# Optimization experiments

Hardware: AMD Instinct MI355X
Metric: run time of the kernel (lower is better)

## Reference

```python
import jax, jax.numpy as jnp
import numpy as np
from jax import lax

DN = ('NCHW', 'OIHW', 'NCHW')

def _edge_bank():
    # All eight fixed stencils embedded in 5x5 (3x3 kernels zero-padded to center),
    # equivalent to the original per-kernel SAME conv. Order matches torch.cat order:
    # sobel_x, sobel_y, diag1, diag2, laplacian, gradient5x5, scharr_x, scharr_y
    k3 = [
        [[-1, 0, 1], [-2, 0, 2], [-1, 0, 1]],            # sobel_x
        [[-1, -2, -1], [0, 0, 0], [1, 2, 1]],            # sobel_y
        [[0, 1, 2], [-1, 0, 1], [-2, -1, 0]],            # diag1
        [[-2, -1, 0], [-1, 0, 1], [0, 1, 2]],            # diag2
        [[0, 1, 0], [1, -4, 1], [0, 1, 0]],              # laplacian
    ]
    g5 = [[-1, -2, 0, 2, 1], [-2, -3, 0, 3, 2], [-3, -4, 0, 4, 3],
          [-2, -3, 0, 3, 2], [-1, -2, 0, 2, 1]]          # gradient5x5
    s3 = [
        [[-3, 0, 3], [-10, 0, 10], [-3, 0, 3]],          # scharr_x
        [[-3, -10, -3], [0, 0, 0], [3, 10, 3]],          # scharr_y
    ]
    ks = []
    for k in k3:
        ks.append(np.pad(np.asarray(k, np.float32), 1))
    ks.append(np.asarray(g5, np.float32))
    for k in s3:
        ks.append(np.pad(np.asarray(k, np.float32), 1))
    return jnp.asarray(np.stack(ks)[:, None, :, :])  # [8,1,5,5]

EDGE_BANK = _edge_bank()

def _conv(x, w, p):
    return lax.conv_general_dilated(x, w, (1, 1), [(p, p), (p, p)], dimension_numbers=DN)

def setup_inputs() -> dict:
    key = jax.random.key(0)
    k = jax.random.split(key, 7)
    x  = jax.random.normal(k[0], (8, 1, 512, 512), jnp.float32)
    w1 = jax.random.normal(k[1], (32, 9, 3, 3), jnp.float32) * 0.05
    b1 = jax.random.normal(k[2], (32,), jnp.float32) * 0.01
    w2 = jax.random.normal(k[3], (16, 32, 3, 3), jnp.float32) * 0.05
    b2 = jax.random.normal(k[4], (16,), jnp.float32) * 0.01
    wr = jax.random.normal(k[5], (16, 1, 1, 1), jnp.float32) * 0.05
    br = jax.random.normal(k[6], (16,), jnp.float32) * 0.01
    return {"x": x, "w1": w1, "b1": b1, "w2": w2, "b2": b2, "wr": wr, "br": br}

def reference(x, w1, b1, w2, b2, wr, br):
    grads = _conv(x, EDGE_BANK, 2)                         # [B,8,H,W] all stencils in one pass
    feats = jnp.concatenate([grads, x], axis=1)            # [B,9,H,W]
    h = jax.nn.relu(_conv(feats, w1, 1) + b1[None, :, None, None])
    fused = jax.nn.relu(_conv(h, w2, 1) + b2[None, :, None, None])
    residual = _conv(x, wr, 0) + br[None, :, None, None]
    return fused + residual
```

## Files before the change

kernel.cpp:

```cpp
#include <hip/hip_runtime.h>
#include <hip/hip_bf16.h>


typedef __attribute__((ext_vector_type(8))) short bf16x8;
typedef __attribute__((ext_vector_type(4))) float f32x4;
typedef unsigned int uint4a __attribute__((ext_vector_type(4), aligned(4)));

#define XS_S 28
#define ST_S 580

#define WS_A2   5120
#define WS_SB   9728
#define WS_FLT  5120
#define WS_WEFF 12800
#define WS_A2I  14848
#define WS_XA   20480
#define XB_OFF  2097152
#define WS_BYTES 38912
#define WS_FULL  8429568u

__device__ const float EB[9][5][5] = {
 {{0,0,0,0,0},{0,-1,0,1,0},{0,-2,0,2,0},{0,-1,0,1,0},{0,0,0,0,0}},
 {{0,0,0,0,0},{0,-1,-2,-1,0},{0,0,0,0,0},{0,1,2,1,0},{0,0,0,0,0}},
 {{0,0,0,0,0},{0,0,1,2,0},{0,-1,0,1,0},{0,-2,-1,0,0},{0,0,0,0,0}},
 {{0,0,0,0,0},{0,-2,-1,0,0},{0,-1,0,1,0},{0,0,1,2,0},{0,0,0,0,0}},
 {{0,0,0,0,0},{0,0,1,0,0},{0,1,-4,1,0},{0,0,1,0,0},{0,0,0,0,0}},
 {{-1,-2,0,2,1},{-2,-3,0,3,2},{-3,-4,0,4,3},{-2,-3,0,3,2},{-1,-2,0,2,1}},
 {{0,0,0,0,0},{0,-3,0,3,0},{0,-10,0,10,0},{0,-3,0,3,0},{0,0,0,0,0}},
 {{0,0,0,0,0},{0,-3,-10,-3,0},{0,0,0,0,0},{0,3,10,3,0},{0,0,0,0,0}},
 {{0,0,0,0,0},{0,0,0,0,0},{0,0,1,0,0},{0,0,0,0,0},{0,0,0,0,0}},
};

__device__ __forceinline__ unsigned short f2bf(float f) {
    union { float f; unsigned u; } v; v.f = f;
    unsigned u = v.u + 0x7fffu + ((v.u >> 16) & 1u);
    return (unsigned short)(u >> 16);
}
__device__ __forceinline__ unsigned pk2(float lo, float hi) {
    __hip_bfloat162 h = __float22bfloat162_rn(make_float2(lo, hi));
    return *reinterpret_cast<unsigned*>(&h);
}

__device__ __forceinline__ float weff_tap(const float* __restrict__ w1,
                                          int oc, int dy, int dx) {
    float s = 0.f;
    for (int ch = 0; ch < 9; ++ch)
        for (int ty = 0; ty < 3; ++ty)
            for (int tx = 0; tx < 3; ++tx) {
                int sy = dy - ty, sx = dx - tx;
                if (sy >= 0 && sy < 5 && sx >= 0 && sx < 5)
                    s += w1[(oc * 9 + ch) * 9 + ty * 3 + tx] * EB[ch][sy][sx];
            }
    return s;
}

__global__ __launch_bounds__(256) void setup_all(
    const float* __restrict__ x,
    const float* __restrict__ w1, const float* __restrict__ b1,
    const float* __restrict__ w2, const float* __restrict__ b2,
    const float* __restrict__ wr, const float* __restrict__ br,
    short* __restrict__ ws, int do_cvt)
{
    const int tid = threadIdx.x;
    if (blockIdx.x != 0) {
        const int j0 = ((blockIdx.x - 1) * 256 + tid) * 8;
        float4 va = *reinterpret_cast<const float4*>(&x[j0]);
        float4 vb = *reinterpret_cast<const float4*>(&x[j0 + 4]);
        float xn = (j0 + 8 < 2097152) ? x[j0 + 8] : 0.f;
        uint4 A; A.x = pk2(va.x, va.y); A.y = pk2(va.z, va.w);
        A.z = pk2(vb.x, vb.y); A.w = pk2(vb.z, vb.w);
        uint4 B; B.x = pk2(va.y, va.z); B.y = pk2(va.w, vb.x);
        B.z = pk2(vb.y, vb.z); B.w = pk2(vb.w, xn);
        *reinterpret_cast<uint4*>(&ws[WS_XA + j0]) = A;
        *reinterpret_cast<uint4*>(&ws[WS_XA + XB_OFF + j0]) = B;
        return;
    }

    __shared__ float w1s[2592];
    __shared__ float w2s[4608];
    __shared__ float ebs[225];
    for (int i = tid; i < 2592; i += 256) w1s[i] = w1[i];
    for (int i = tid; i < 4608; i += 256) w2s[i] = w2[i];
    if (tid < 225) ebs[tid] = ((const float*)EB)[tid];
    __syncthreads();

    for (int idx = tid; idx < 5120; idx += 256) {
        int i = idx & 7, lane = (idx >> 3) & 63, rest = idx >> 9;
        int mt = rest / 5, ks = rest - 5 * mt;
        int n = lane & 15, lg = lane >> 4;
        int k = 32 * ks + 8 * lg + i;
        int g = k >> 4, ch = k & 15;
        float w = (g < 9 && ch < 9) ? w1s[(mt * 16 + n) * 81 + ch * 9 + g] : 0.f;
        ws[idx] = (short)f2bf(w);
    }
    for (int idx = tid; idx < 4608; idx += 256) {
        int i = idx & 7, lane = (idx >> 3) & 63, ks = idx >> 9;
        int n = lane & 15, lg = lane >> 4;
        ws[WS_A2 + idx] = (short)f2bf(w2s[n * 288 + (8 * lg + i) * 9 + ks]);
    }
    for (int idx = tid; idx < 4608; idx += 256) {
        int i = idx & 7, lane = (idx >> 3) & 63, ks = idx >> 9;
        int n = lane & 15, lg = lane >> 4;
        int ic = ((i & 1) << 4) | (lg << 2) | ((i >> 1) & 3);
        ws[WS_A2I + idx] = (short)f2bf(w2s[n * 288 + ic * 9 + ks]);
    }
    for (int idx = tid; idx < 512; idx += 256) {
        int i = idx & 7, lane = idx >> 3;
        int n = lane & 15, lg = lane >> 4;
        int k = 8 * lg + i;
        float v = (k < 25 && n < 9) ? ebs[n * 25 + k] : 0.f;
        ws[WS_SB + idx] = (short)f2bf(v);
    }
    for (int idx = tid; idx < 2048; idx += 256) {
        int i = idx & 7, lane = (idx >> 3) & 63, rest = idx >> 9;
        int mt = rest >> 1, ks = rest & 1;
        int n = lane & 15, lg = lane >> 4;
        int dy = 4 * ks + lg, dx = i;
        float s = 0.f;
        if (dy < 7 && dx < 7) {
            int oc = mt * 16 + n;
            for (int ch = 0; ch < 9; ++ch)
                for (int ty = 0; ty < 3; ++ty) {
                    int sy = dy - ty;
                    if (sy < 0 || sy >= 5) continue;
                    for (int tx = 0; tx < 3; ++tx) {
                        int sx = dx - tx;
                        if (sx >= 0 && sx < 5)
                            s += w1s[(oc * 9 + ch) * 9 + ty * 3 + tx] * ebs[ch * 25 + sy * 5 + sx];
                    }
                }
        }
        ws[WS_WEFF + idx] = (short)f2bf(s);
    }
    if (tid < 64) {
        int lg = tid >> 4;
        float* wf = (float*)ws + WS_FLT + tid * 20;
        for (int r = 0; r < 4; ++r) {
            wf[r]      = b1[lg * 4 + r];
            wf[4 + r]  = b1[16 + lg * 4 + r];
            wf[8 + r]  = b2[lg * 4 + r];
            wf[12 + r] = wr[lg * 4 + r];
            wf[16 + r] = br[lg * 4 + r];
        }
    }
    (void)do_cvt;
}

__global__ __launch_bounds__(256, 4) void edge_main(
    const float* __restrict__ x, const short* __restrict__ ws,
    float* __restrict__ out)
{
    __shared__ long long pool[39936 / 8];
    const int tid  = threadIdx.x;
    const int lane = tid & 63;
    const int wave = tid >> 6;
    const int n    = lane & 15;
    const int lg   = lane >> 4;
    const int id   = blockIdx.x;

    if (id >= 992) {
        short* hsS   = (short*)pool;
        float* stage = (float*)pool;
        const int id2 = id - 992;
        const int bx = (id2 & 15) * 32;
        const int rem = id2 >> 4;
        const int by = (rem % 30 + 1) * 16;
        const int b  = rem / 30;
        const float* xb = x + ((size_t)b << 18);
        const short* xab = ws + WS_XA + b * 262144;

        bf16x8 wa[2][2], a2[9];
        float b1v[2][4], b2v[4], wrv[4], brv[4];
#pragma unroll
        for (int mt = 0; mt < 2; ++mt)
#pragma unroll
            for (int ks = 0; ks < 2; ++ks)
                wa[mt][ks] = *reinterpret_cast<const bf16x8*>(
                    &ws[WS_WEFF + ((mt * 2 + ks) * 64 + lane) * 8]);
#pragma unroll
        for (int ks = 0; ks < 9; ++ks)
            a2[ks] = *reinterpret_cast<const bf16x8*>(&ws[WS_A2I + (ks * 64 + lane) * 8]);
        {
            const float* wf = (const float*)ws + WS_FLT + lane * 20;
            f32x4 t0 = *reinterpret_cast<const f32x4*>(wf);
            f32x4 t1 = *reinterpret_cast<const f32x4*>(wf + 4);
            f32x4 t2 = *reinterpret_cast<const f32x4*>(wf + 8);
            f32x4 t3 = *reinterpret_cast<const f32x4*>(wf + 12);
            f32x4 t4 = *reinterpret_cast<const f32x4*>(wf + 16);
#pragma unroll
            for (int r = 0; r < 4; ++r) {
                b1v[0][r] = t0[r]; b1v[1][r] = t1[r];
                b2v[r] = t2[r]; wrv[r] = t3[r]; brv[r] = t4[r];
            }
        }

#pragma unroll 2
        for (int t = wave; t < 39; t += 4) {
            int p  = t * 16 + n;
            int r1 = p / 34, c1 = p - 34 * r1;
            int gxb = bx - 4 + c1; gxb = gxb < 0 ? 0 : (gxb > 504 ? 504 : gxb);
            const int off = (by - 4 + r1) * 512 + gxb;
            const short* basep = (gxb & 1) ? (xab + XB_OFF + off - 1) : (xab + off);
            f32x4 acc0 = {0.f,0.f,0.f,0.f}, acc1 = {0.f,0.f,0.f,0.f};
#pragma unroll
            for (int ks = 0; ks < 2; ++ks) {
                const int dy = 4 * ks + lg;
                uint4a u = *reinterpret_cast<const uint4a*>(basep + dy * 512);
                bf16x8 bv = __builtin_bit_cast(bf16x8, u);
                acc0 = __builtin_amdgcn_mfma_f32_16x16x32_bf16(wa[0][ks], bv, acc0, 0, 0, 0);
                acc1 = __builtin_amdgcn_mfma_f32_16x16x32_bf16(wa[1][ks], bv, acc1, 0, 0, 0);
            }
            float h0 = fmaxf(acc0[0] + b1v[0][0], 0.f), g0 = fmaxf(acc1[0] + b1v[1][0], 0.f);
            float h1 = fmaxf(acc0[1] + b1v[0][1], 0.f), g1 = fmaxf(acc1[1] + b1v[1][1], 0.f);
            float h2 = fmaxf(acc0[2] + b1v[0][2], 0.f), g2 = fmaxf(acc1[2] + b1v[1][2], 0.f);
            float h3 = fmaxf(acc0[3] + b1v[0][3], 0.f), g3 = fmaxf(acc1[3] + b1v[1][3], 0.f);
            uint4 W;
            W.x = pk2(h0, g0); W.y = pk2(h1, g1); W.z = pk2(h2, g2); W.w = pk2(h3, g3);
            const int grp = lg ^ (p & 3) ^ ((p >> 2) & 3);
            *reinterpret_cast<uint4*>(&hsS[p * 32 + grp * 8]) = W;
        }
        __syncthreads();

        const int q0 = wave >> 1;
        const int hh = wave & 1;
        f32x4 oreg[8];
#pragma unroll
        for (int j = 0; j < 2; ++j) {
            const int q = q0 + 2 * j;
            f32x4 acc[4] = {{0.f,0.f,0.f,0.f},{0.f,0.f,0.f,0.f},
                            {0.f,0.f,0.f,0.f},{0.f,0.f,0.f,0.f}};
#pragma unroll
            for (int rr = 0; rr < 6; ++rr) {
                const int pxb = (4 * q + rr) * 34 + 16 * hh + n;
#pragma unroll
                for (int dx = 0; dx < 3; ++dx) {
                    const int px = pxb + dx;
                    const int grp = lg ^ (px & 3) ^ ((px >> 2) & 3);
                    bf16x8 hf = *reinterpret_cast<const bf16x8*>(&hsS[px * 32 + grp * 8]);
#pragma unroll
                    for (int o = 0; o < 4; ++o) {
                        const int dy = rr - o;
                        if (dy >= 0 && dy < 3)
                            acc[o] = __builtin_amdgcn_mfma_f32_16x16x32_bf16(
                                a2[dy * 3 + dx], hf, acc[o], 0, 0, 0);
                    }
                }
            }
#pragma unroll
            for (int o = 0; o < 4; ++o) {
                const int oy = 4 * q + o;
                float xv = xb[((size_t)(by + oy) << 9) + bx + 16 * hh + n];
                f32x4 ov;
#pragma unroll
                for (int r = 0; r < 4; ++r)
                    ov[r] = fmaxf(acc[o][r] + b2v[r], 0.f) + wrv[r] * xv + brv[r];
                oreg[4 * j + o] = ov;
            }
        }
        __syncthreads();

#pragma unroll
        for (int j = 0; j < 2; ++j) {
            const int q = q0 + 2 * j;
#pragma unroll
            for (int o = 0; o < 4; ++o)
#pragma unroll
                for (int r = 0; r < 4; ++r)
                    stage[(lg * 4 + r) * ST_S + (4 * q + o) * 36 + 16 * hh + n] = oreg[4 * j + o][r];
        }
        __syncthreads();
#pragma unroll
        for (int k = 0; k < 8; ++k) {
            int idx = k * 256 + tid;
            int c   = idx & 7;
            int row = (idx >> 3) & 15;
            int oc  = idx >> 7;
            if ((bx == 0 && c < 4) || (bx == 480 && c >= 4)) continue;
            f32x4 v = *reinterpret_cast<const f32x4*>(&stage[oc * ST_S + row * 36 + 4 * c]);
            __builtin_nontemporal_store(v, reinterpret_cast<f32x4*>(
                &out[(((size_t)b * 16 + oc) * 512 + (by + row)) * 512 + bx + 4 * c]));
        }
        return;
    }

    {
        short* fs2 = (short*)pool;
        short* hs4 = (short*)pool + 6400;
        short* xs  = (short*)pool + 16768;

        const int b = id / 124;
        int t4 = id - b * 124, tx, ty;
        if      (t4 < 32) { tx = t4;      ty = 0;  }
        else if (t4 < 64) { tx = t4 - 32; ty = 31; }
        else if (t4 < 94) { tx = 0;       ty = t4 - 63; }
        else              { tx = 31;      ty = t4 - 93; }
        const int bx = tx * 16, by = ty * 16;

        for (int i = tid; i < 576; i += 256) {
            int r = i / 24, c = i % 24;
            int gy = by - 4 + r, gx = bx - 4 + c;
            float v = 0.f;
            if (gy >= 0 && gy < 512 && gx >= 0 && gx < 512)
                v = x[((size_t)b * 512 + gy) * 512 + gx];
            __hip_bfloat16 h = __float2bfloat16(v);
            xs[r * XS_S + c] = *reinterpret_cast<short*>(&h);
        }

        bf16x8 a1[2][5], a2[9], sb;
        float b1v[2][4], b2v[4], wrv[4], brv[4];
#pragma unroll
        for (int mt = 0; mt < 2; ++mt)
#pragma unroll
            for (int ks = 0; ks < 5; ++ks)
                a1[mt][ks] = *reinterpret_cast<const bf16x8*>(&ws[((mt * 5 + ks) * 64 + lane) * 8]);
#pragma unroll
        for (int ks = 0; ks < 9; ++ks)
            a2[ks] = *reinterpret_cast<const bf16x8*>(&ws[WS_A2 + (ks * 64 + lane) * 8]);
        sb = *reinterpret_cast<const bf16x8*>(&ws[WS_SB + lane * 8]);
        {
            const float* wf = (const float*)ws + WS_FLT + lane * 20;
            f32x4 t0 = *reinterpret_cast<const f32x4*>(wf);
            f32x4 t1 = *reinterpret_cast<const f32x4*>(wf + 4);
            f32x4 t2 = *reinterpret_cast<const f32x4*>(wf + 8);
            f32x4 t3 = *reinterpret_cast<const f32x4*>(wf + 12);
            f32x4 t4 = *reinterpret_cast<const f32x4*>(wf + 16);
#pragma unroll
            for (int r = 0; r < 4; ++r) {
                b1v[0][r] = t0[r]; b1v[1][r] = t1[r];
                b2v[r] = t2[r]; wrv[r] = t3[r]; brv[r] = t4[r];
            }
        }

        int toff[8];
#pragma unroll
        for (int i = 0; i < 8; ++i) {
            int k = 8 * lg + i;
            int t = k < 25 ? k : 24;
            toff[i] = (t / 5) * XS_S + (t % 5);
        }
        int boff[5];
#pragma unroll
        for (int ks = 0; ks < 5; ++ks) {
            int g = 2 * ks + (lg >> 1); if (g > 8) g = 8;
            int dy = g / 3, dx = g - 3 * dy;
            boff[ks] = (lg & 1) * 3200 + (dy * 20 + dx) * 8;
        }

        __syncthreads();

        for (int t = wave; t < 25; t += 4) {
            int px = t * 16 + n;
            int r = px / 20, c = px - 20 * r;
            const short* base = &xs[r * XS_S + c];
            bf16x8 bv;
#pragma unroll
            for (int i = 0; i < 8; ++i) bv[i] = base[toff[i]];
            f32x4 f = {0.f, 0.f, 0.f, 0.f};
            f = __builtin_amdgcn_mfma_f32_16x16x32_bf16(sb, bv, f, 0, 0, 0);
            int fy = by + r - 2, fx = bx + c - 2;
            float m = (fy >= 0 && fy < 512 && fx >= 0 && fx < 512) ? 1.f : 0.f;
            uint2 wv;
            wv.x = pk2(f[0] * m, f[1] * m);
            wv.y = pk2(f[2] * m, f[3] * m);
            *reinterpret_cast<uint2*>(&fs2[((lg >> 1) * 400 + px) * 8 + 4 * (lg & 1)]) = wv;
        }
        __syncthreads();

        for (int t = wave; t < 21; t += 4) {
            int p  = t * 16 + n;
            int pc = p < 323 ? p : 323;
            int r1 = pc / 18, c1 = pc - 18 * r1;
            int base = (r1 * 20 + c1) * 8;
            f32x4 acc0 = {0.f,0.f,0.f,0.f}, acc1 = {0.f,0.f,0.f,0.f};
#pragma unroll
            for (int ks = 0; ks < 5; ++ks) {
                bf16x8 bf = *reinterpret_cast<const bf16x8*>(&fs2[base + boff[ks]]);
                acc0 = __builtin_amdgcn_mfma_f32_16x16x32_bf16(a1[0][ks], bf, acc0, 0, 0, 0);
                acc1 = __builtin_amdgcn_mfma_f32_16x16x32_bf16(a1[1][ks], bf, acc1, 0, 0, 0);
            }
            if (p < 324) {
                int hy = by - 1 + r1, hx = bx - 1 + c1;
                float m = (hy >= 0 && hy < 512 && hx >= 0 && hx < 512) ? 1.f : 0.f;
                uint2 W0;
                W0.x = pk2(fmaxf(acc0[0] + b1v[0][0], 0.f) * m, fmaxf(acc0[1] + b1v[0][1], 0.f) * m);
                W0.y = pk2(fmaxf(acc0[2] + b1v[0][2], 0.f) * m, fmaxf(acc0[3] + b1v[0][3], 0.f) * m);
                *reinterpret_cast<uint2*>(&hs4[((lg >> 1) * 324 + p) * 8 + 4 * (lg & 1)]) = W0;
                uint2 W1;
                W1.x = pk2(fmaxf(acc1[0] + b1v[1][0], 0.f) * m, fmaxf(acc1[1] + b1v[1][1], 0.f) * m);
                W1.y = pk2(fmaxf(acc1[2] + b1v[1][2], 0.f) * m, fmaxf(acc1[3] + b1v[1][3], 0.f) * m);
                *reinterpret_cast<uint2*>(&hs4[((2 + (lg >> 1)) * 324 + p) * 8 + 4 * (lg & 1)]) = W1;
            }
        }
        __syncthreads();

        const int hbase = lg * 324 * 8;
#pragma unroll
        for (int j = 0; j < 4; ++j) {
            int oy = wave + 4 * j;
            f32x4 acc = {0.f,0.f,0.f,0.f};
#pragma unroll
            for (int ks = 0; ks < 9; ++ks) {
                const int dy = ks / 3, dx = ks - 3 * (ks / 3);
                bf16x8 hf = *reinterpret_cast<const bf16x8*>(
                    &hs4[hbase + ((oy + dy) * 18 + n + dx) * 8]);
                acc = __builtin_amdgcn_mfma_f32_16x16x32_bf16(a2[ks], hf, acc, 0, 0, 0);
            }
            __hip_bfloat16 xh = *reinterpret_cast<const __hip_bfloat16*>(&xs[(oy + 4) * XS_S + n + 4]);
            float xv = __bfloat162float(xh);
            float* op = out + (((size_t)(b * 16 + lg * 4) * 512 + (by + oy)) * 512) + bx + n;
#pragma unroll
            for (int r = 0; r < 4; ++r) {
                float o = fmaxf(acc[r] + b2v[r], 0.f) + wrv[r] * xv + brv[r];
                *op = o;
                op += 262144;
            }
        }
    }
}

template<bool USE_WS>
__global__ __launch_bounds__(256, 4) void edge_interior4(
    const float* __restrict__ x,  const float* __restrict__ w1, const float* __restrict__ b1,
    const float* __restrict__ w2, const float* __restrict__ b2,
    const float* __restrict__ wr, const float* __restrict__ br,
    const short* __restrict__ ws, float* __restrict__ out)
{
    __shared__ long long pool[39168 / 8];
    short* hsS   = (short*)pool;
    float* stage = (float*)pool;

    const int tid  = threadIdx.x;
    const int lane = tid & 63;
    const int wave = tid >> 6;
    const int n    = lane & 15;
    const int lg   = lane >> 4;
    const int bx = blockIdx.x * 32;
    const int by = (blockIdx.y + 1) * 16;
    const int b  = blockIdx.z;
    const float* xb = x + ((size_t)b << 18);

    bf16x8 wa[2][2], a2[9];
    float b1v[2][4], b2v[4], wrv[4], brv[4];
    if (USE_WS) {
#pragma unroll
        for (int mt = 0; mt < 2; ++mt)
#pragma unroll
            for (int ks = 0; ks < 2; ++ks)
                wa[mt][ks] = *reinterpret_cast<const bf16x8*>(
                    &ws[WS_WEFF + ((mt * 2 + ks) * 64 + lane) * 8]);
#pragma unroll
        for (int ks = 0; ks < 9; ++ks)
            a2[ks] = *reinterpret_cast<const bf16x8*>(&ws[WS_A2I + (ks * 64 + lane) * 8]);
        const float* wf = (const float*)ws + WS_FLT + lane * 20;
        f32x4 t0 = *reinterpret_cast<const f32x4*>(wf);
        f32x4 t1 = *reinterpret_cast<const f32x4*>(wf + 4);
        f32x4 t2 = *reinterpret_cast<const f32x4*>(wf + 8);
        f32x4 t3 = *reinterpret_cast<const f32x4*>(wf + 12);
        f32x4 t4 = *reinterpret_cast<const f32x4*>(wf + 16);
#pragma unroll
        for (int r = 0; r < 4; ++r) {
            b1v[0][r] = t0[r]; b1v[1][r] = t1[r];
            b2v[r] = t2[r]; wrv[r] = t3[r]; brv[r] = t4[r];
        }
    } else {
#pragma unroll
        for (int mt = 0; mt < 2; ++mt)
#pragma unroll
            for (int ks = 0; ks < 2; ++ks)
#pragma unroll
                for (int i = 0; i < 8; ++i) {
                    int dy = 4 * ks + lg, dx = i;
                    float s = (dy < 7 && dx < 7) ? weff_tap(w1, mt * 16 + n, dy, dx) : 0.f;
                    wa[mt][ks][i] = (short)f2bf(s);
                }
#pragma unroll
        for (int ks = 0; ks < 9; ++ks)
#pragma unroll
            for (int i = 0; i < 8; ++i) {
                int ic = ((i & 1) << 4) | (lg << 2) | ((i >> 1) & 3);
                a2[ks][i] = (short)f2bf(w2[(n * 32 + ic) * 9 + ks]);
            }
#pragma unroll
        for (int r = 0; r < 4; ++r) {
            b1v[0][r] = b1[lg * 4 + r]; b1v[1][r] = b1[16 + lg * 4 + r];
            b2v[r] = b2[lg * 4 + r]; wrv[r] = wr[lg * 4 + r]; brv[r] = br[lg * 4 + r];
        }
    }

    for (int t = wave; t < 39; t += 4) {
        int p  = t * 16 + n;
        int pc = p < 611 ? p : 611;
        int r1 = pc / 34, c1 = pc - 34 * r1;
        int gxb = bx - 4 + c1; gxb = gxb < 0 ? 0 : (gxb > 504 ? 504 : gxb);
        const int gyb = by - 4 + r1;
        f32x4 acc0 = {0.f,0.f,0.f,0.f}, acc1 = {0.f,0.f,0.f,0.f};
#pragma unroll
        for (int ks = 0; ks < 2; ++ks) {
            const int dy = 4 * ks + lg;
            bf16x8 bv = {0,0,0,0,0,0,0,0};
            if (dy < 7) {
                const float* xp = xb + ((size_t)(gyb + dy) << 9) + gxb;
                uint4 u;
                u.x = pk2(xp[0], xp[1]); u.y = pk2(xp[2], xp[3]);
                u.z = pk2(xp[4], xp[5]); u.w = pk2(xp[6], xp[7]);
                bv = *reinterpret_cast<bf16x8*>(&u);
            }
            acc0 = __builtin_amdgcn_mfma_f32_16x16x32_bf16(wa[0][ks], bv, acc0, 0, 0, 0);
            acc1 = __builtin_amdgcn_mfma_f32_16x16x32_bf16(wa[1][ks], bv, acc1, 0, 0, 0);
        }
        if (p < 612) {
            float h0 = fmaxf(acc0[0] + b1v[0][0], 0.f), g0 = fmaxf(acc1[0] + b1v[1][0], 0.f);
            float h1 = fmaxf(acc0[1] + b1v[0][1], 0.f), g1 = fmaxf(acc1[1] + b1v[1][1], 0.f);
            float h2 = fmaxf(acc0[2] + b1v[0][2], 0.f), g2 = fmaxf(acc1[2] + b1v[1][2], 0.f);
            float h3 = fmaxf(acc0[3] + b1v[0][3], 0.f), g3 = fmaxf(acc1[3] + b1v[1][3], 0.f);
            uint4 W;
            W.x = pk2(h0, g0); W.y = pk2(h1, g1); W.z = pk2(h2, g2); W.w = pk2(h3, g3);
            const int grp = lg ^ (p & 3) ^ ((p >> 2) & 3);
            *reinterpret_cast<uint4*>(&hsS[p * 32 + grp * 8]) = W;
        }
    }
    __syncthreads();

    const int q0 = wave >> 1;
    const int hh = wave & 1;
    f32x4 oreg[8];
#pragma unroll
    for (int j = 0; j < 2; ++j) {
        const int q = q0 + 2 * j;
        f32x4 acc[4] = {{0.f,0.f,0.f,0.f},{0.f,0.f,0.f,0.f},
                        {0.f,0.f,0.f,0.f},{0.f,0.f,0.f,0.f}};
#pragma unroll
        for (int rr = 0; rr < 6; ++rr) {
            const int pxb = (4 * q + rr) * 34 + 16 * hh + n;
#pragma unroll
            for (int dx = 0; dx < 3; ++dx) {
                const int px = pxb + dx;
                const int grp = lg ^ (px & 3) ^ ((px >> 2) & 3);
                bf16x8 hf = *reinterpret_cast<const bf16x8*>(&hsS[px * 32 + grp * 8]);
#pragma unroll
                for (int o = 0; o < 4; ++o) {
                    const int dy = rr - o;
                    if (dy >= 0 && dy < 3)
                        acc[o] = __builtin_amdgcn_mfma_f32_16x16x32_bf16(
                            a2[dy * 3 + dx], hf, acc[o], 0, 0, 0);
                }
            }
        }
#pragma unroll
        for (int o = 0; o < 4; ++o) {
            const int oy = 4 * q + o;
            float xv = xb[((size_t)(by + oy) << 9) + bx + 16 * hh + n];
            f32x4 ov;
#pragma unroll
            for (int r = 0; r < 4; ++r)
                ov[r] = fmaxf(acc[o][r] + b2v[r], 0.f) + wrv[r] * xv + brv[r];
            oreg[4 * j + o] = ov;
        }
    }
    __syncthreads();

#pragma unroll
    for (int j = 0; j < 2; ++j) {
        const int q = q0 + 2 * j;
#pragma unroll
        for (int o = 0; o < 4; ++o)
#pragma unroll
            for (int r = 0; r < 4; ++r)
                stage[(lg * 4 + r) * 576 + (4 * q + o) * 36 + 16 * hh + n] = oreg[4 * j + o][r];
    }
    __syncthreads();

#pragma unroll
    for (int k = 0; k < 8; ++k) {
        int idx = k * 256 + tid;
        int c   = idx & 7;
        int row = (idx >> 3) & 15;
        int oc  = idx >> 7;
        f32x4 v = *reinterpret_cast<const f32x4*>(&stage[oc * 576 + row * 36 + 4 * c]);
        __builtin_nontemporal_store(v, reinterpret_cast<f32x4*>(
            &out[(((size_t)b * 16 + oc) * 512 + (by + row)) * 512 + bx + 4 * c]));
    }
}

template<bool USE_WS>
__global__ __launch_bounds__(256, 4) void edge_border(
    const float* __restrict__ x,  const float* __restrict__ w1, const float* __restrict__ b1,
    const float* __restrict__ w2, const float* __restrict__ b2,
    const float* __restrict__ wr, const float* __restrict__ br,
    const short* __restrict__ ws, float* __restrict__ out)
{
    __shared__ short fs2[2 * 400 * 8];
    __shared__ short hs4[4 * 324 * 8];
    __shared__ short xs[24 * XS_S];

    const int tid  = threadIdx.x;
    const int lane = tid & 63;
    const int wave = tid >> 6;
    const int n    = lane & 15;
    const int lg   = lane >> 4;

    int idx = blockIdx.x, tx, ty;
    if      (idx < 32) { tx = idx;      ty = 0;  }
    else if (idx < 64) { tx = idx - 32; ty = 31; }
    else if (idx < 94) { tx = 0;        ty = idx - 63; }
    else               { tx = 31;       ty = idx - 93; }
    const int bx = tx * 16, by = ty * 16, b = blockIdx.z;

    for (int i = tid; i < 576; i += 256) {
        int r = i / 24, c = i % 24;
        int gy = by - 4 + r, gx = bx - 4 + c;
        float v = 0.f;
        if (gy >= 0 && gy < 512 && gx >= 0 && gx < 512) v = x[((size_t)b * 512 + gy) * 512 + gx];
        __hip_bfloat16 h = __float2bfloat16(v);
        xs[r * XS_S + c] = *reinterpret_cast<short*>(&h);
    }

    bf16x8 a1[2][5], a2[9], sb;
    float b1v[2][4], b2v[4], wrv[4], brv[4];
    if (USE_WS) {
#pragma unroll
        for (int mt = 0; mt < 2; ++mt)
#pragma unroll
            for (int ks = 0; ks < 5; ++ks)
                a1[mt][ks] = *reinterpret_cast<const bf16x8*>(&ws[((mt * 5 + ks) * 64 + lane) * 8]);
#pragma unroll
        for (int ks = 0; ks < 9; ++ks)
            a2[ks] = *reinterpret_cast<const bf16x8*>(&ws[WS_A2 + (ks * 64 + lane) * 8]);
        sb = *reinterpret_cast<const bf16x8*>(&ws[WS_SB + lane * 8]);
        const float* wf = (const float*)ws + WS_FLT + lane * 20;
        f32x4 t0 = *reinterpret_cast<const f32x4*>(wf);
        f32x4 t1 = *reinterpret_cast<const f32x4*>(wf + 4);
        f32x4 t2 = *reinterpret_cast<const f32x4*>(wf + 8);
        f32x4 t3 = *reinterpret_cast<const f32x4*>(wf + 12);
        f32x4 t4 = *reinterpret_cast<const f32x4*>(wf + 16);
#pragma unroll
        for (int r = 0; r < 4; ++r) {
            b1v[0][r] = t0[r]; b1v[1][r] = t1[r];
            b2v[r] = t2[r]; wrv[r] = t3[r]; brv[r] = t4[r];
        }
    } else {
#pragma unroll
        for (int mt = 0; mt < 2; ++mt)
#pragma unroll
            for (int ks = 0; ks < 5; ++ks)
#pragma unroll
                for (int i = 0; i < 8; ++i) {
                    int k = 32 * ks + 8 * lg + i;
                    int g = k >> 4, ch = k & 15;
                    float w = (g < 9 && ch < 9) ? w1[(mt * 16 + n) * 81 + ch * 9 + g] : 0.f;
                    a1[mt][ks][i] = (short)f2bf(w);
                }
#pragma unroll
        for (int ks = 0; ks < 9; ++ks)
#pragma unroll
            for (int i = 0; i < 8; ++i)
                a2[ks][i] = (short)f2bf(w2[n * 288 + (8 * lg + i) * 9 + ks]);
#pragma unroll
        for (int i = 0; i < 8; ++i) {
            int k = 8 * lg + i;
            float v = (k < 25 && n < 9) ? EB[n][k / 5][k % 5] : 0.f;
            sb[i] = (short)f2bf(v);
        }
#pragma unroll
        for (int r = 0; r < 4; ++r) {
            b1v[0][r] = b1[lg * 4 + r]; b1v[1][r] = b1[16 + lg * 4 + r];
            b2v[r] = b2[lg * 4 + r]; wrv[r] = wr[lg * 4 + r]; brv[r] = br[lg * 4 + r];
        }
    }

    int toff[8];
#pragma unroll
    for (int i = 0; i < 8; ++i) {
        int k = 8 * lg + i;
        int t = k < 25 ? k : 24;
        toff[i] = (t / 5) * XS_S + (t % 5);
    }
    int boff[5];
#pragma unroll
    for (int ks = 0; ks < 5; ++ks) {
        int g = 2 * ks + (lg >> 1); if (g > 8) g = 8;
        int dy = g / 3, dx = g - 3 * dy;
        boff[ks] = (lg & 1) * 3200 + (dy * 20 + dx) * 8;
    }

    __syncthreads();

    for (int t = wave; t < 25; t += 4) {
        int px = t * 16 + n;
        int r = px / 20, c = px - 20 * r;
        const short* base = &xs[r * XS_S + c];
        bf16x8 bv;
#pragma unroll
        for (int i = 0; i < 8; ++i) bv[i] = base[toff[i]];
        f32x4 f = {0.f, 0.f, 0.f, 0.f};
        f = __builtin_amdgcn_mfma_f32_16x16x32_bf16(sb, bv, f, 0, 0, 0);
        int fy = by + r - 2, fx = bx + c - 2;
        float m = (fy >= 0 && fy < 512 && fx >= 0 && fx < 512) ? 1.f : 0.f;
        uint2 wv;
        wv.x = pk2(f[0] * m, f[1] * m);
        wv.y = pk2(f[2] * m, f[3] * m);
        *reinterpret_cast<uint2*>(&fs2[((lg >> 1) * 400 + px) * 8 + 4 * (lg & 1)]) = wv;
    }
    __syncthreads();

    for (int t = wave; t < 21; t += 4) {
        int p  = t * 16 + n;
        int pc = p < 323 ? p : 323;
        int r1 = pc / 18, c1 = pc - 18 * r1;
        int base = (r1 * 20 + c1) * 8;
        f32x4 acc0 = {0.f,0.f,0.f,0.f}, acc1 = {0.f,0.f,0.f,0.f};
#pragma unroll
        for (int ks = 0; ks < 5; ++ks) {
            bf16x8 bf = *reinterpret_cast<const bf16x8*>(&fs2[base + boff[ks]]);
            acc0 = __builtin_amdgcn_mfma_f32_16x16x32_bf16(a1[0][ks], bf, acc0, 0, 0, 0);
            acc1 = __builtin_amdgcn_mfma_f32_16x16x32_bf16(a1[1][ks], bf, acc1, 0, 0, 0);
        }
        if (p < 324) {
            int hy = by - 1 + r1, hx = bx - 1 + c1;
            float m = (hy >= 0 && hy < 512 && hx >= 0 && hx < 512) ? 1.f : 0.f;
            uint2 W0;
            W0.x = pk2(fmaxf(acc0[0] + b1v[0][0], 0.f) * m, fmaxf(acc0[1] + b1v[0][1], 0.f) * m);
            W0.y = pk2(fmaxf(acc0[2] + b1v[0][2], 0.f) * m, fmaxf(acc0[3] + b1v[0][3], 0.f) * m);
            *reinterpret_cast<uint2*>(&hs4[((lg >> 1) * 324 + p) * 8 + 4 * (lg & 1)]) = W0;
            uint2 W1;
            W1.x = pk2(fmaxf(acc1[0] + b1v[1][0], 0.f) * m, fmaxf(acc1[1] + b1v[1][1], 0.f) * m);
            W1.y = pk2(fmaxf(acc1[2] + b1v[1][2], 0.f) * m, fmaxf(acc1[3] + b1v[1][3], 0.f) * m);
            *reinterpret_cast<uint2*>(&hs4[((2 + (lg >> 1)) * 324 + p) * 8 + 4 * (lg & 1)]) = W1;
        }
    }
    __syncthreads();

    const int hbase = lg * 324 * 8;
#pragma unroll
    for (int j = 0; j < 4; ++j) {
        int oy = wave + 4 * j;
        f32x4 acc = {0.f,0.f,0.f,0.f};
#pragma unroll
        for (int ks = 0; ks < 9; ++ks) {
            const int dy = ks / 3, dx = ks - 3 * (ks / 3);
            bf16x8 hf = *reinterpret_cast<const bf16x8*>(
                &hs4[hbase + ((oy + dy) * 18 + n + dx) * 8]);
            acc = __builtin_amdgcn_mfma_f32_16x16x32_bf16(a2[ks], hf, acc, 0, 0, 0);
        }
        __hip_bfloat16 xh = *reinterpret_cast<const __hip_bfloat16*>(&xs[(oy + 4) * XS_S + n + 4]);
        float xv = __bfloat162float(xh);
        float* op = out + (((size_t)(b * 16 + lg * 4) * 512 + (by + oy)) * 512) + bx + n;
#pragma unroll
        for (int r = 0; r < 4; ++r) {
            float o = fmaxf(acc[r] + b2v[r], 0.f) + wrv[r] * xv + brv[r];
            *op = o;
            op += 262144;
        }
    }
}

extern "C" void kernel_launch(void* const* d_in, const int* in_sizes, int n_in,
                              void* d_out, int out_size, void* d_ws, size_t ws_size,
                              hipStream_t stream) {
    const float* x  = (const float*)d_in[0];
    const float* w1 = (const float*)d_in[1];
    const float* b1 = (const float*)d_in[2];
    const float* w2 = (const float*)d_in[3];
    const float* b2 = (const float*)d_in[4];
    const float* wr = (const float*)d_in[5];
    const float* br = (const float*)d_in[6];
    float* out = (float*)d_out;
    short* ws = (short*)d_ws;

    dim3 block(256);
    if (ws_size >= WS_FULL) {
        hipLaunchKernelGGL(setup_all, dim3(1025), block, 0, stream,
                           x, w1, b1, w2, b2, wr, br, ws, 1);
        hipLaunchKernelGGL(edge_main, dim3(4832), block, 0, stream, x, ws, out);
    } else if (ws_size >= WS_BYTES) {
        hipLaunchKernelGGL(setup_all, dim3(1), block, 0, stream,
                           x, w1, b1, w2, b2, wr, br, ws, 0);
        hipLaunchKernelGGL(edge_interior4<true>, dim3(16, 30, 8), block, 0, stream,
                           x, w1, b1, w2, b2, wr, br, ws, out);
        hipLaunchKernelGGL(edge_border<true>, dim3(124, 1, 8), block, 0, stream,
                           x, w1, b1, w2, b2, wr, br, ws, out);
    } else {
        hipLaunchKernelGGL(edge_interior4<false>, dim3(16, 30, 8), block, 0, stream,
                           x, w1, b1, w2, b2, wr, br, ws, out);
        hipLaunchKernelGGL(edge_border<false>, dim3(124, 1, 8), block, 0, stream,
                           x, w1, b1, w2, b2, wr, br, ws, out);
    }
}
```

Before: 92.11 us.

## Halve tile height to cut LDS and raise occupancy, write outputs directly

Interior and border tiles shrink from 16 to 8 rows, which halves the shared-memory pool and doubles the grid. Launch bounds are raised so more blocks fit per CU. The LDS staging pass and its two barriers before the output store are removed, and each lane now writes its results straight to global memory with strided scalar stores. In exchange, the relative halo overhead of the conv1 recompute grows and the stores become less coalesced.

```diff
diff --git a/kernel.cpp b/kernel.cpp
--- a/kernel.cpp
+++ b/kernel.cpp
@@ -7,7 +7,6 @@
 typedef unsigned int uint4a __attribute__((ext_vector_type(4), aligned(4)));
 
 #define XS_S 28
-#define ST_S 580
 
 #define WS_A2   5120
 #define WS_SB   9728
@@ -146,11 +145,11 @@
     (void)do_cvt;
 }
 
-__global__ __launch_bounds__(256, 4) void edge_main(
+__global__ __launch_bounds__(256, 7) void edge_main(
     const float* __restrict__ x, const short* __restrict__ ws,
     float* __restrict__ out)
 {
-    __shared__ long long pool[39936 / 8];
+    __shared__ long long pool[22528 / 8];
     const int tid  = threadIdx.x;
     const int lane = tid & 63;
     const int wave = tid >> 6;
@@ -158,14 +157,13 @@
     const int lg   = lane >> 4;
     const int id   = blockIdx.x;
 
-    if (id >= 992) {
-        short* hsS   = (short*)pool;
-        float* stage = (float*)pool;
-        const int id2 = id - 992;
+    if (id >= 1984) {
+        short* hsS = (short*)pool;
+        const int id2 = id - 1984;
         const int bx = (id2 & 15) * 32;
         const int rem = id2 >> 4;
-        const int by = (rem % 30 + 1) * 16;
-        const int b  = rem / 30;
+        const int by = 16 + (rem % 60) * 8;
+        const int b  = rem / 60;
         const float* xb = x + ((size_t)b << 18);
         const short* xab = ws + WS_XA + b * 262144;
 
@@ -195,7 +193,7 @@
         }
 
 #pragma unroll 2
-        for (int t = wave; t < 39; t += 4) {
+        for (int t = wave; t < 22; t += 4) {
             int p  = t * 16 + n;
             int r1 = p / 34, c1 = p - 34 * r1;
             int gxb = bx - 4 + c1; gxb = gxb < 0 ? 0 : (gxb > 504 ? 504 : gxb);
@@ -223,80 +221,57 @@
 
         const int q0 = wave >> 1;
         const int hh = wave & 1;
-        f32x4 oreg[8];
-#pragma unroll
-        for (int j = 0; j < 2; ++j) {
-            const int q = q0 + 2 * j;
-            f32x4 acc[4] = {{0.f,0.f,0.f,0.f},{0.f,0.f,0.f,0.f},
-                            {0.f,0.f,0.f,0.f},{0.f,0.f,0.f,0.f}};
-#pragma unroll
-            for (int rr = 0; rr < 6; ++rr) {
-                const int pxb = (4 * q + rr) * 34 + 16 * hh + n;
-#pragma unroll
-                for (int dx = 0; dx < 3; ++dx) {
-                    const int px = pxb + dx;
-                    const int grp = lg ^ (px & 3) ^ ((px >> 2) & 3);
-                    bf16x8 hf = *reinterpret_cast<const bf16x8*>(&hsS[px * 32 + grp * 8]);
-#pragma unroll
-                    for (int o = 0; o < 4; ++o) {
-                        const int dy = rr - o;
-                        if (dy >= 0 && dy < 3)
-                            acc[o] = __builtin_amdgcn_mfma_f32_16x16x32_bf16(
-                                a2[dy * 3 + dx], hf, acc[o], 0, 0, 0);
-                    }
+        f32x4 acc[4] = {{0.f,0.f,0.f,0.f},{0.f,0.f,0.f,0.f},
+                        {0.f,0.f,0.f,0.f},{0.f,0.f,0.f,0.f}};
+#pragma unroll
+        for (int rr = 0; rr < 6; ++rr) {
+            const int pxb = (4 * q0 + rr) * 34 + 16 * hh + n;
+#pragma unroll
+            for (int dx = 0; dx < 3; ++dx) {
+                const int px = pxb + dx;
+                const int grp = lg ^ (px & 3) ^ ((px >> 2) & 3);
+                bf16x8 hf = *reinterpret_cast<const bf16x8*>(&hsS[px * 32 + grp * 8]);
+#pragma unroll
+                for (int o = 0; o < 4; ++o) {
+                    const int dy = rr - o;
+                    if (dy >= 0 && dy < 3)
+                        acc[o] = __builtin_amdgcn_mfma_f32_16x16x32_bf16(
+                            a2[dy * 3 + dx], hf, acc[o], 0, 0, 0);
                 }
             }
+        }
+        const bool skip = (bx == 0 && hh == 0) || (bx == 480 && hh == 1);
+        if (!skip) {
 #pragma unroll
             for (int o = 0; o < 4; ++o) {
-                const int oy = 4 * q + o;
+                const int oy = 4 * q0 + o;
                 float xv = xb[((size_t)(by + oy) << 9) + bx + 16 * hh + n];
-                f32x4 ov;
-#pragma unroll
-                for (int r = 0; r < 4; ++r)
-                    ov[r] = fmaxf(acc[o][r] + b2v[r], 0.f) + wrv[r] * xv + brv[r];
-                oreg[4 * j + o] = ov;
-            }
-        }
-        __syncthreads();
-
-#pragma unroll
-        for (int j = 0; j < 2; ++j) {
-            const int q = q0 + 2 * j;
-#pragma unroll
-            for (int o = 0; o < 4; ++o)
-#pragma unroll
-                for (int r = 0; r < 4; ++r)
-                    stage[(lg * 4 + r) * ST_S + (4 * q + o) * 36 + 16 * hh + n] = oreg[4 * j + o][r];
-        }
-        __syncthreads();
-#pragma unroll
-        for (int k = 0; k < 8; ++k) {
-            int idx = k * 256 + tid;
-            int c   = idx & 7;
-            int row = (idx >> 3) & 15;
-            int oc  = idx >> 7;
-            if ((bx == 0 && c < 4) || (bx == 480 && c >= 4)) continue;
-            f32x4 v = *reinterpret_cast<const f32x4*>(&stage[oc * ST_S + row * 36 + 4 * c]);
-            __builtin_nontemporal_store(v, reinterpret_cast<f32x4*>(
-                &out[(((size_t)b * 16 + oc) * 512 + (by + row)) * 512 + bx + 4 * c]));
+                float* op = out + (((size_t)(b * 16 + lg * 4) * 512 + (by + oy)) * 512)
+                          + bx + 16 * hh + n;
+#pragma unroll
+                for (int r = 0; r < 4; ++r) {
+                    float ov = fmaxf(acc[o][r] + b2v[r], 0.f) + wrv[r] * xv + brv[r];
+                    *op = ov;
+                    op += 262144;
+                }
+            }
         }
         return;
     }
 
     {
         short* fs2 = (short*)pool;
-        short* hs4 = (short*)pool + 6400;
-        short* xs  = (short*)pool + 16768;
-
-        const int b = id / 124;
-        int t4 = id - b * 124, tx, ty;
-        if      (t4 < 32) { tx = t4;      ty = 0;  }
-        else if (t4 < 64) { tx = t4 - 32; ty = 31; }
-        else if (t4 < 94) { tx = 0;       ty = t4 - 63; }
-        else              { tx = 31;      ty = t4 - 93; }
-        const int bx = tx * 16, by = ty * 16;
-
-        for (int i = tid; i < 576; i += 256) {
+        short* hs4 = (short*)pool + 3840;
+        short* xs  = (short*)pool + 9984;
+
+        const int b = id / 248;
+        int t4 = id - b * 248, bx, by;
+        if      (t4 < 64)  { bx = (t4 & 31) * 16;        by = (t4 >> 5) * 8; }
+        else if (t4 < 128) { int tt = t4 - 64;  bx = (tt & 31) * 16; by = 496 + (tt >> 5) * 8; }
+        else if (t4 < 188) { int tt = t4 - 128; bx = 0;   by = 16 + tt * 8; }
+        else               { int tt = t4 - 188; bx = 496; by = 16 + tt * 8; }
+
+        for (int i = tid; i < 384; i += 256) {
             int r = i / 24, c = i % 24;
             int gy = by - 4 + r, gx = bx - 4 + c;
             float v = 0.f;
@@ -323,11 +298,11 @@
             f32x4 t1 = *reinterpret_cast<const f32x4*>(wf + 4);
             f32x4 t2 = *reinterpret_cast<const f32x4*>(wf + 8);
             f32x4 t3 = *reinterpret_cast<const f32x4*>(wf + 12);
-            f32x4 t4 = *reinterpret_cast<const f32x4*>(wf + 16);
+            f32x4 t4v = *reinterpret_cast<const f32x4*>(wf + 16);
 #pragma unroll
             for (int r = 0; r < 4; ++r) {
                 b1v[0][r] = t0[r]; b1v[1][r] = t1[r];
-                b2v[r] = t2[r]; wrv[r] = t3[r]; brv[r] = t4[r];
+                b2v[r] = t2[r]; wrv[r] = t3[r]; brv[r] = t4v[r];
             }
         }
 
@@ -343,12 +318,12 @@
         for (int ks = 0; ks < 5; ++ks) {
             int g = 2 * ks + (lg >> 1); if (g > 8) g = 8;
             int dy = g / 3, dx = g - 3 * dy;
-            boff[ks] = (lg & 1) * 3200 + (dy * 20 + dx) * 8;
+            boff[ks] = (lg & 1) * 1920 + (dy * 20 + dx) * 8;
         }
 
         __syncthreads();
 
-        for (int t = wave; t < 25; t += 4) {
+        for (int t = wave; t < 15; t += 4) {
             int px = t * 16 + n;
             int r = px / 20, c = px - 20 * r;
             const short* base = &xs[r * XS_S + c];
@@ -362,14 +337,13 @@
             uint2 wv;
             wv.x = pk2(f[0] * m, f[1] * m);
             wv.y = pk2(f[2] * m, f[3] * m);
-            *reinterpret_cast<uint2*>(&fs2[((lg >> 1) * 400 + px) * 8 + 4 * (lg & 1)]) = wv;
+            *reinterpret_cast<uint2*>(&fs2[((lg >> 1) * 240 + px) * 8 + 4 * (lg & 1)]) = wv;
         }
         __syncthreads();
 
-        for (int t = wave; t < 21; t += 4) {
+        for (int t = wave; t < 12; t += 4) {
             int p  = t * 16 + n;
-            int pc = p < 323 ? p : 323;
-            int r1 = pc / 18, c1 = pc - 18 * r1;
+            int r1 = p / 18, c1 = p - 18 * r1;
             int base = (r1 * 20 + c1) * 8;
             f32x4 acc0 = {0.f,0.f,0.f,0.f}, acc1 = {0.f,0.f,0.f,0.f};
 #pragma unroll
@@ -378,24 +352,22 @@
                 acc0 = __builtin_amdgcn_mfma_f32_16x16x32_bf16(a1[0][ks], bf, acc0, 0, 0, 0);
                 acc1 = __builtin_amdgcn_mfma_f32_16x16x32_bf16(a1[1][ks], bf, acc1, 0, 0, 0);
             }
-            if (p < 324) {
-                int hy = by - 1 + r1, hx = bx - 1 + c1;
-                float m = (hy >= 0 && hy < 512 && hx >= 0 && hx < 512) ? 1.f : 0.f;
-                uint2 W0;
-                W0.x = pk2(fmaxf(acc0[0] + b1v[0][0], 0.f) * m, fmaxf(acc0[1] + b1v[0][1], 0.f) * m);
-                W0.y = pk2(fmaxf(acc0[2] + b1v[0][2], 0.f) * m, fmaxf(acc0[3] + b1v[0][3], 0.f) * m);
-                *reinterpret_cast<uint2*>(&hs4[((lg >> 1) * 324 + p) * 8 + 4 * (lg & 1)]) = W0;
-                uint2 W1;
-                W1.x = pk2(fmaxf(acc1[0] + b1v[1][0], 0.f) * m, fmaxf(acc1[1] + b1v[1][1], 0.f) * m);
-                W1.y = pk2(fmaxf(acc1[2] + b1v[1][2], 0.f) * m, fmaxf(acc1[3] + b1v[1][3], 0.f) * m);
-                *reinterpret_cast<uint2*>(&hs4[((2 + (lg >> 1)) * 324 + p) * 8 + 4 * (lg & 1)]) = W1;
-            }
+            int hy = by - 1 + r1, hx = bx - 1 + c1;
+            float m = (hy >= 0 && hy < 512 && hx >= 0 && hx < 512) ? 1.f : 0.f;
+            uint2 W0;
+            W0.x = pk2(fmaxf(acc0[0] + b1v[0][0], 0.f) * m, fmaxf(acc0[1] + b1v[0][1], 0.f) * m);
+            W0.y = pk2(fmaxf(acc0[2] + b1v[0][2], 0.f) * m, fmaxf(acc0[3] + b1v[0][3], 0.f) * m);
+            *reinterpret_cast<uint2*>(&hs4[((lg >> 1) * 192 + p) * 8 + 4 * (lg & 1)]) = W0;
+            uint2 W1;
+            W1.x = pk2(fmaxf(acc1[0] + b1v[1][0], 0.f) * m, fmaxf(acc1[1] + b1v[1][1], 0.f) * m);
+            W1.y = pk2(fmaxf(acc1[2] + b1v[1][2], 0.f) * m, fmaxf(acc1[3] + b1v[1][3], 0.f) * m);
+            *reinterpret_cast<uint2*>(&hs4[((2 + (lg >> 1)) * 192 + p) * 8 + 4 * (lg & 1)]) = W1;
         }
         __syncthreads();
 
-        const int hbase = lg * 324 * 8;
-#pragma unroll
-        for (int j = 0; j < 4; ++j) {
+        const int hbase = lg * 192 * 8;
+#pragma unroll
+        for (int j = 0; j < 2; ++j) {
             int oy = wave + 4 * j;
             f32x4 acc = {0.f,0.f,0.f,0.f};
 #pragma unroll
@@ -441,16 +413,35 @@
 
     bf16x8 wa[2][2], a2[9];
     float b1v[2][4], b2v[4], wrv[4], brv[4];
-    if (USE_WS) {
-#pragma unroll
-        for (int mt = 0; mt < 2; ++mt)
-#pragma unroll
-            for (int ks = 0; ks < 2; ++ks)
+#pragma unroll
+    for (int mt = 0; mt < 2; ++mt)
+#pragma unroll
+        for (int ks = 0; ks < 2; ++ks) {
+            if (USE_WS) {
                 wa[mt][ks] = *reinterpret_cast<const bf16x8*>(
                     &ws[WS_WEFF + ((mt * 2 + ks) * 64 + lane) * 8]);
-#pragma unroll
-        for (int ks = 0; ks < 9; ++ks)
+            } else {
+#pragma unroll
+                for (int i = 0; i < 8; ++i) {
+                    int dy = 4 * ks + lg, dx = i;
+                    float s = (dy < 7 && dx < 7) ? weff_tap(w1, mt * 16 + n, dy, dx) : 0.f;
+                    wa[mt][ks][i] = (short)f2bf(s);
+                }
+            }
+        }
+#pragma unroll
+    for (int ks = 0; ks < 9; ++ks) {
+        if (USE_WS) {
             a2[ks] = *reinterpret_cast<const bf16x8*>(&ws[WS_A2I + (ks * 64 + lane) * 8]);
+        } else {
+#pragma unroll
+            for (int i = 0; i < 8; ++i) {
+                int ic = ((i & 1) << 4) | (lg << 2) | ((i >> 1) & 3);
+                a2[ks][i] = (short)f2bf(w2[(n * 32 + ic) * 9 + ks]);
+            }
+        }
+    }
+    if (USE_WS) {
         const float* wf = (const float*)ws + WS_FLT + lane * 20;
         f32x4 t0 = *reinterpret_cast<const f32x4*>(wf);
         f32x4 t1 = *reinterpret_cast<const f32x4*>(wf + 4);
@@ -463,23 +454,6 @@
             b2v[r] = t2[r]; wrv[r] = t3[r]; brv[r] = t4[r];
         }
     } else {
-#pragma unroll
-        for (int mt = 0; mt < 2; ++mt)
-#pragma unroll
-            for (int ks = 0; ks < 2; ++ks)
-#pragma unroll
-                for (int i = 0; i < 8; ++i) {
-                    int dy = 4 * ks + lg, dx = i;
-                    float s = (dy < 7 && dx < 7) ? weff_tap(w1, mt * 16 + n, dy, dx) : 0.f;
-                    wa[mt][ks][i] = (short)f2bf(s);
-                }
-#pragma unroll
-        for (int ks = 0; ks < 9; ++ks)
-#pragma unroll
-            for (int i = 0; i < 8; ++i) {
-                int ic = ((i & 1) << 4) | (lg << 2) | ((i >> 1) & 3);
-                a2[ks][i] = (short)f2bf(w2[(n * 32 + ic) * 9 + ks]);
-            }
 #pragma unroll
         for (int r = 0; r < 4; ++r) {
             b1v[0][r] = b1[lg * 4 + r]; b1v[1][r] = b1[16 + lg * 4 + r];
@@ -771,7 +745,7 @@
     if (ws_size >= WS_FULL) {
         hipLaunchKernelGGL(setup_all, dim3(1025), block, 0, stream,
                            x, w1, b1, w2, b2, wr, br, ws, 1);
-        hipLaunchKernelGGL(edge_main, dim3(4832), block, 0, stream, x, ws, out);
+        hipLaunchKernelGGL(edge_main, dim3(9664), block, 0, stream, x, ws, out);
     } else if (ws_size >= WS_BYTES) {
         hipLaunchKernelGGL(setup_all, dim3(1), block, 0, stream,
                            x, w1, b1, w2, b2, wr, br, ws, 0);
```

Result: slower. 176.0 us (+91.1%).
